# Kernel tuning notes

Hardware: AMD Instinct MI355X
Metric: run time of the kernel (lower is better)

## Reference

```python
import jax, jax.numpy as jnp
import numpy as np

N = 50000          # num nodes
E_RAND = 1_600_000 # random edges (self-loops appended -> E = E_RAND + N)
H, D = 4, 32       # heads, per-head dim
HID = H * D        # 128
L = 3              # num GATv2 layers
NODE_DIM, GRAPH_DIM = 64, 32
EPS = 1e-5


def setup_inputs() -> dict:
    key = jax.random.key(0)
    ks = jax.random.split(key, 24)
    s = 0.05  # param init scale
    node_feats = jax.random.normal(ks[0], (N, NODE_DIM), jnp.float32)
    graph_feats = jax.random.normal(ks[1], (GRAPH_DIM,), jnp.float32)
    # random edges + self loops (mirrors dgl.add_self_loop in forward)
    src = jnp.concatenate([jax.random.randint(ks[2], (E_RAND,), 0, N), jnp.arange(N)]).astype(jnp.int32)
    dst = jnp.concatenate([jax.random.randint(ks[3], (E_RAND,), 0, N), jnp.arange(N)]).astype(jnp.int32)
    p = lambda k, shp: s * jax.random.normal(k, shp, jnp.float32)
    return {
        'node_feats': node_feats, 'graph_feats': graph_feats, 'src': src, 'dst': dst,
        'W_in': p(ks[4], (NODE_DIM, HID)), 'b_in': jnp.zeros((HID,), jnp.float32),
        'W_g': p(ks[5], (GRAPH_DIM, HID)), 'b_g': jnp.zeros((HID,), jnp.float32),
        'W_src': p(ks[6], (L, HID, HID)), 'b_src': jnp.zeros((L, HID), jnp.float32),
        'W_dst': p(ks[7], (L, HID, HID)), 'b_dst': jnp.zeros((L, HID), jnp.float32),
        'attn': p(ks[8], (L, H, D)),
        'ln_g': jnp.ones((L, HID), jnp.float32), 'ln_b': jnp.zeros((L, HID), jnp.float32),
        'W_f1': p(ks[9], (2 * HID, HID)), 'b_f1': jnp.zeros((HID,), jnp.float32),
        'W_f2': p(ks[10], (HID, HID)), 'b_f2': jnp.zeros((HID,), jnp.float32),
    }


def _layernorm(x, g, b):
    m = jnp.mean(x, -1, keepdims=True)
    v = jnp.mean(jnp.square(x - m), -1, keepdims=True)
    return (x - m) * jax.lax.rsqrt(v + EPS) * g + b


def _gatv2(h, src, dst, Ws, bs, Wd, bd, a):
    # DGL GATv2Conv (share_weights=False, residual identity since in==H*D)
    fs = (h @ Ws + bs).reshape(N, H, D)
    fd = (h @ Wd + bd).reshape(N, H, D)
    e = jax.nn.leaky_relu(fs[src] + fd[dst], 0.2)          # [E,H,D]
    logits = jnp.einsum('ehd,hd->eh', e, a)                # [E,H]
    mx = jax.ops.segment_max(logits, dst, num_segments=N)  # [N,H]
    ex = jnp.exp(logits - mx[dst])
    den = jax.ops.segment_sum(ex, dst, num_segments=N)     # [N,H]
    alpha = ex / den[dst]                                  # edge softmax
    out = jax.ops.segment_sum(alpha[:, :, None] * fs[src], dst, num_segments=N)
    return out.reshape(N, HID) + h                         # identity residual


def reference(node_feats, graph_feats, src, dst, W_in, b_in, W_g, b_g,
              W_src, b_src, W_dst, b_dst, attn, ln_g, ln_b,
              W_f1, b_f1, W_f2, b_f2):
    h = node_feats @ W_in + b_in                # [N,HID]
    graph_h = graph_feats @ W_g + b_g           # [HID]
    for l in range(L):
        h_new = _gatv2(h, src, dst, W_src[l], b_src[l], W_dst[l], b_dst[l], attn[l])
        h = jax.nn.relu(_layernorm(h + h_new, ln_g[l], ln_b[l]))  # dropout eval-mode
    pooled = jnp.mean(h, axis=0)                # [HID]
    combined = jnp.concatenate([pooled, graph_h])
    graph_emb = jax.nn.relu(combined @ W_f1 + b_f1) @ W_f2 + b_f2
    return graph_emb, h
```

## Files before the change

### kernel.cpp

```cpp
#include <hip/hip_runtime.h>

typedef unsigned short ushort_t;
typedef unsigned int   uint_t;
typedef unsigned char  uchar_t;
typedef __attribute__((ext_vector_type(8))) __bf16 bf16x8;
typedef __attribute__((ext_vector_type(4))) float   f32x4;

__device__ __forceinline__ float bl(uint_t u){ return __uint_as_float(u<<16); }
__device__ __forceinline__ float bh(uint_t u){ return __uint_as_float(u & 0xffff0000u); }
__device__ __forceinline__ ushort_t f2b(float f){
  uint_t x = __float_as_uint(f);
  return (ushort_t)((x + 0x7fffu + ((x>>16)&1u)) >> 16);
}
__device__ __forceinline__ uint_t pack2(float a, float b){
  return (uint_t)f2b(a) | ((uint_t)f2b(b) << 16);
}

__device__ __forceinline__ float row_reduce16(float p){
  float t;
  t = __uint_as_float(__builtin_amdgcn_update_dpp(0, __float_as_uint(p), 0x121, 0xf, 0xf, true)); p += t;
  t = __uint_as_float(__builtin_amdgcn_update_dpp(0, __float_as_uint(p), 0x122, 0xf, 0xf, true)); p += t;
  t = __uint_as_float(__builtin_amdgcn_update_dpp(0, __float_as_uint(p), 0x124, 0xf, 0xf, true)); p += t;
  t = __uint_as_float(__builtin_amdgcn_update_dpp(0, __float_as_uint(p), 0x128, 0xf, 0xf, true)); p += t;
  return p;
}

#define NBK 128
#define PBLK 256

__global__ __launch_bounds__(256) void k_fuse_a(
    const float* __restrict__ Wsrc, const float* __restrict__ Wdst,
    ushort_t* __restrict__ WB,
    const int* __restrict__ dst, int* __restrict__ bhist, int E, int epb,
    float* __restrict__ pooled)
{
  int blk = blockIdx.x;
  if (blk < 48) {
    int t = blk*256 + threadIdx.x;
    int l = t >> 12;
    int rem = t & 4095;
    int ct = rem >> 8;
    int kc = (rem >> 6) & 3;
    int lane = rem & 63;
    int n = ct*16 + (lane & 15);
    int kbase = kc*32 + (lane >> 4)*8;
    const float* Wp; int nn;
    if (n < 128) { Wp = Wsrc + l*16384; nn = n; }
    else         { Wp = Wdst + l*16384; nn = n - 128; }
    uint4 o;
    o.x = pack2(Wp[(kbase+0)*128+nn], Wp[(kbase+1)*128+nn]);
    o.y = pack2(Wp[(kbase+2)*128+nn], Wp[(kbase+3)*128+nn]);
    o.z = pack2(Wp[(kbase+4)*128+nn], Wp[(kbase+5)*128+nn]);
    o.w = pack2(Wp[(kbase+6)*128+nn], Wp[(kbase+7)*128+nn]);
    *(uint4*)&WB[(size_t)t * 8] = o;
  } else if (blk < 304) {
    __shared__ int lh[NBK];
    int b2 = blk - 48, t = threadIdx.x;
    if (t < NBK) lh[t] = 0;
    __syncthreads();
    int s = b2*epb, e = s + epb; if (e > E) e = E;
    for (int i = s + t; i < e; i += 256)
      atomicAdd(&lh[dst[i] >> 9], 1);
    __syncthreads();
    if (t < NBK) bhist[t*PBLK + b2] = lh[t];
  } else {
    if (threadIdx.x < 128) pooled[threadIdx.x] = 0.f;
  }
}

__global__ __launch_bounds__(1024) void k_scan2(
    const int* __restrict__ bhist, int* __restrict__ gOff,
    int* __restrict__ bucketOff, int E)
{
  __shared__ int sums[1024];
  int tid = threadIdx.x;
  int s0 = tid * 32;
  int local = 0;
  #pragma unroll
  for (int i = 0; i < 32; ++i) local += bhist[s0 + i];
  sums[tid] = local;
  __syncthreads();
  for (int off = 1; off < 1024; off <<= 1) {
    int v = (tid >= off) ? sums[tid - off] : 0;
    __syncthreads();
    sums[tid] += v;
    __syncthreads();
  }
  int run = (tid == 0) ? 0 : sums[tid - 1];
  #pragma unroll
  for (int i = 0; i < 32; ++i) { gOff[s0 + i] = run; run += bhist[s0 + i]; }
  __syncthreads();
  if (tid < NBK) bucketOff[tid] = gOff[tid*PBLK];
  if (tid == NBK) bucketOff[NBK] = E;
}

__global__ __launch_bounds__(256) void k_fuse_b(
    const int* __restrict__ src, const int* __restrict__ dst,
    const int* __restrict__ gOff, uint_t* __restrict__ part, int E, int epb,
    const float* __restrict__ nf, const float* __restrict__ W,
    const float* __restrict__ b, ushort_t* __restrict__ HB, int N)
{
  __shared__ int loff[NBK];
  __shared__ float sA[64*64];
  if (blockIdx.x < PBLK) {
    int blk = blockIdx.x, t = threadIdx.x;
    if (t < NBK) loff[t] = gOff[t*PBLK + blk];
    __syncthreads();
    int s = blk*epb, e = s + epb; if (e > E) e = E;
    for (int i = s + t; i < e; i += 256) {
      int d = dst[i];
      int bb = d >> 9;
      int p = atomicAdd(&loff[bb], 1);
      part[p] = (uint_t)src[i] | ((uint_t)(d & 511) << 16);
    }
  } else {
    int row0 = (blockIdx.x - PBLK) * 64;
    int tid = threadIdx.x;
    {
      int q = tid;
      #pragma unroll
      for (int j = 0; j < 4; ++j, q += 256) {
        int r = q >> 4;
        int c = (q & 15) << 2;
        float4 v = make_float4(0.f,0.f,0.f,0.f);
        if (row0 + r < N) v = *(const float4*)&nf[(size_t)(row0 + r)*64 + c];
        *(float4*)&sA[r*64 + c] = v;
      }
    }
    __syncthreads();
    int cg = tid & 15, rg = tid >> 4;
    int c0 = cg * 8;
    float acc[4][8];
    #pragma unroll
    for (int i = 0; i < 4; ++i)
      #pragma unroll
      for (int j = 0; j < 8; ++j) acc[i][j] = 0.f;
    for (int k = 0; k < 64; ++k) {
      float4 wa = *(const float4*)&W[k*128 + c0];
      float4 wb = *(const float4*)&W[k*128 + c0 + 4];
      float w[8] = {wa.x,wa.y,wa.z,wa.w,wb.x,wb.y,wb.z,wb.w};
      float hv[4];
      #pragma unroll
      for (int i = 0; i < 4; ++i) hv[i] = sA[(rg*4 + i)*64 + k];
      #pragma unroll
      for (int i = 0; i < 4; ++i)
        #pragma unroll
        for (int j = 0; j < 8; ++j) acc[i][j] += hv[i]*w[j];
    }
    float4 b1 = *(const float4*)&b[c0];
    float4 b2 = *(const float4*)&b[c0 + 4];
    float bb[8] = {b1.x,b1.y,b1.z,b1.w,b2.x,b2.y,b2.z,b2.w};
    #pragma unroll
    for (int i = 0; i < 4; ++i) {
      int row = row0 + rg*4 + i;
      if (row < N) {
        uint4 hb;
        hb.x = pack2(acc[i][0]+bb[0], acc[i][1]+bb[1]);
        hb.y = pack2(acc[i][2]+bb[2], acc[i][3]+bb[3]);
        hb.z = pack2(acc[i][4]+bb[4], acc[i][5]+bb[5]);
        hb.w = pack2(acc[i][6]+bb[6], acc[i][7]+bb[7]);
        *(uint4*)&HB[(size_t)row*128 + c0] = hb;
      }
    }
  }
}

__global__ __launch_bounds__(512) void k_csr(
    const uint_t* __restrict__ part, const int* __restrict__ bucketOff,
    int* __restrict__ rowp, int* __restrict__ csrc32, int N, int E)
{
  __shared__ int lcnt[512];
  __shared__ int lpos[512];
  int b = blockIdx.x, t = threadIdx.x;
  int base = b << 9;
  int cnt = N - base; if (cnt > 512) cnt = 512;
  lcnt[t] = 0;
  __syncthreads();
  int s = bucketOff[b], e = bucketOff[b + 1];
  for (int i = s + t; i < e; i += 512)
    atomicAdd(&lcnt[part[i] >> 16], 1);
  __syncthreads();
  int v = lcnt[t];
  lpos[t] = v;
  __syncthreads();
  for (int off = 1; off < 512; off <<= 1) {
    int u = (t >= off) ? lpos[t - off] : 0;
    __syncthreads();
    lpos[t] += u;
    __syncthreads();
  }
  int rp = s + lpos[t] - v;
  if (t < cnt) rowp[base + t] = rp;
  if (b == 0 && t == 0) rowp[N] = E;
  __syncthreads();
  lpos[t] = rp;
  __syncthreads();
  for (int i = s + t; i < e; i += 512) {
    uint_t pr = part[i];
    int p = atomicAdd(&lpos[pr >> 16], 1);
    csrc32[p] = (int)((pr & 0xffffu) << 7);
  }
}

__global__ __launch_bounds__(256) void k_gemm_mfma(
    const ushort_t* __restrict__ HB, const ushort_t* __restrict__ WB,
    const float* __restrict__ bsrc, const float* __restrict__ bdst,
    uchar_t* __restrict__ FS8, ushort_t* __restrict__ FD, int N)
{
  int m0 = blockIdx.x * 32;
  int tid = threadIdx.x;
  int w = tid >> 6, lane = tid & 63;
  int lrow = lane & 15, lk = lane >> 4;

  bf16x8 a[2][4];
  #pragma unroll
  for (int rt = 0; rt < 2; ++rt) {
    int row = m0 + rt*16 + lrow;
    if (row > N-1) row = N-1;
    #pragma unroll
    for (int kc = 0; kc < 4; ++kc)
      a[rt][kc] = *(const bf16x8*)&HB[(size_t)row*128 + kc*32 + lk*8];
  }

  #pragma unroll
  for (int c = 0; c < 4; ++c) {
    int ct = w*4 + c;
    int n = ct*16 + lrow;
    bf16x8 bfr[4];
    #pragma unroll
    for (int kc = 0; kc < 4; ++kc)
      bfr[kc] = *(const bf16x8*)&WB[((size_t)(ct*4 + kc)*64 + lane) * 8];
    if (ct < 8) {
      float bias = bsrc[n];
      #pragma unroll
      for (int rt = 0; rt < 2; ++rt) {
        f32x4 acc = {0.f, 0.f, 0.f, 0.f};
        #pragma unroll
        for (int kc = 0; kc < 4; ++kc)
          acc = __builtin_amdgcn_mfma_f32_16x16x32_bf16(a[rt][kc], bfr[kc], acc, 0, 0, 0);
        int r = m0 + rt*16 + lk*4;
        int w01 = __builtin_amdgcn_cvt_pk_fp8_f32(acc[0]+bias, acc[1]+bias, 0, false);
        int w23 = __builtin_amdgcn_cvt_pk_fp8_f32(acc[2]+bias, acc[3]+bias, 0, false);
        if (r     < N) FS8[(size_t)(r    )*128 + n] = (uchar_t)(w01);
        if (r + 1 < N) FS8[(size_t)(r + 1)*128 + n] = (uchar_t)(w01 >> 8);
        if (r + 2 < N) FS8[(size_t)(r + 2)*128 + n] = (uchar_t)(w23);
        if (r + 3 < N) FS8[(size_t)(r + 3)*128 + n] = (uchar_t)(w23 >> 8);
      }
    } else {
      int nn = n & 127;
      float bias = bdst[nn];
      #pragma unroll
      for (int rt = 0; rt < 2; ++rt) {
        f32x4 acc = {0.f, 0.f, 0.f, 0.f};
        #pragma unroll
        for (int kc = 0; kc < 4; ++kc)
          acc = __builtin_amdgcn_mfma_f32_16x16x32_bf16(a[rt][kc], bfr[kc], acc, 0, 0, 0);
        #pragma unroll
        for (int reg = 0; reg < 4; ++reg) {
          int row = m0 + rt*16 + lk*4 + reg;
          if (row < N) FD[(size_t)row*128 + nn] = f2b(acc[reg] + bias);
        }
      }
    }
  }
}

__global__ __launch_bounds__(256) void k_edge(
    const uchar_t* __restrict__ FS8, const ushort_t* __restrict__ FD,
    ushort_t* __restrict__ HB, float* __restrict__ H,
    const int* __restrict__ rowp, const int* __restrict__ csrc32,
    const float* __restrict__ attn, const float* __restrict__ lng,
    const float* __restrict__ lnb, int last, int N)
{
  int node = __builtin_amdgcn_readfirstlane(blockIdx.x * 4 + (threadIdx.x >> 6));
  if (node >= N) return;
  int lane = threadIdx.x & 63;
  int g = lane >> 4;
  int c = lane & 15;
  int cb = c << 3;

  float fdv[8], av6[8], av4[8];
  {
    uint4 fdu = *(const uint4*)((const char*)FD + node*256 + (cb << 1));
    fdv[0]=bl(fdu.x); fdv[1]=bh(fdu.x); fdv[2]=bl(fdu.y); fdv[3]=bh(fdu.y);
    fdv[4]=bl(fdu.z); fdv[5]=bh(fdu.z); fdv[6]=bl(fdu.w); fdv[7]=bh(fdu.w);
    float4 a1 = *(const float4*)&attn[cb];
    float4 a2 = *(const float4*)&attn[cb + 4];
    float aa[8] = {a1.x,a1.y,a1.z,a1.w,a2.x,a2.y,a2.z,a2.w};
    #pragma unroll
    for (int k = 0; k < 8; ++k) {
      av6[k] = aa[k] * 0.865617024f;
      av4[k] = aa[k] * 0.577078016f;
    }
  }
  int beg = __builtin_amdgcn_readfirstlane(rowp[node]);
  int end = __builtin_amdgcn_readfirstlane(rowp[node + 1]);
  int deg = end - beg;
  int npair = deg >> 4, ntail = deg & 15;
  int tb = beg + (npair << 4);
  int endm1 = end - 1;

  float den = 0.f;
  float acc[8];
  #pragma unroll
  for (int k = 0; k < 8; ++k) acc[k] = 0.f;

  uint2 a0,a1q,a2q,a3q, b0,b1q,b2q,b3q, t0,t1q,t2q,t3q;

  #define PREF(bu0, bu1, kb) {                                              \
    int s0 = csrc32[(kb) + g];                                              \
    int s1 = csrc32[(kb) + 4 + g];                                          \
    bu0 = *(const uint2*)((const char*)FS8 + s0 + cb);                      \
    bu1 = *(const uint2*)((const char*)FS8 + s1 + cb);                      \
  }

  #define PREFT(bu0, bu1, kb) {                                             \
    int i0 = (kb) + g;     i0 = (i0 < endm1) ? i0 : endm1;                  \
    int i1 = (kb) + 4 + g; i1 = (i1 < endm1) ? i1 : endm1;                  \
    bu0 = *(const uint2*)((const char*)FS8 + csrc32[i0] + cb);              \
    bu1 = *(const uint2*)((const char*)FS8 + csrc32[i1] + cb);              \
  }

  #define QM(u, MASKED, kbq) {                                              \
    float cf[8];                                                            \
    { auto p01 = __builtin_amdgcn_cvt_pk_f32_fp8((int)(u).x, false);        \
      auto p23 = __builtin_amdgcn_cvt_pk_f32_fp8((int)(u).x, true);         \
      auto p45 = __builtin_amdgcn_cvt_pk_f32_fp8((int)(u).y, false);        \
      auto p67 = __builtin_amdgcn_cvt_pk_f32_fp8((int)(u).y, true);         \
      cf[0]=p01[0]; cf[1]=p01[1]; cf[2]=p23[0]; cf[3]=p23[1];               \
      cf[4]=p45[0]; cf[5]=p45[1]; cf[6]=p67[0]; cf[7]=p67[1]; }             \
    float p = 0.f;                                                          \
    _Pragma("unroll")                                                       \
    for (int k = 0; k < 8; ++k) {                                           \
      float x = cf[k] + fdv[k];                                             \
      p = fmaf(x, av6[k], p);                                               \
      p = fmaf(fabsf(x), av4[k], p);                                        \
    }                                                                       \
    p = row_reduce16(p);                                                    \
    float ex = __builtin_amdgcn_exp2f(p);                                   \
    if (MASKED) ex = ((kbq) + g < end) ? ex : 0.f;                          \
    den += ex;                                                              \
    _Pragma("unroll")                                                       \
    for (int k = 0; k < 8; ++k) acc[k] = fmaf(ex, cf[k], acc[k]);           \
  }

  if (ntail) { PREFT(t0, t1q, tb) PREFT(t2q, t3q, tb + 8) }
  if (npair) {
    PREF(a0, a1q, beg) PREF(a2q, a3q, beg + 8)
    int rem2 = npair, kb = beg + 16;
    for (;;) {
      if (rem2 > 1) { PREF(b0, b1q, kb) PREF(b2q, b3q, kb + 8) }
      QM(a0, 0, 0) QM(a1q, 0, 0) QM(a2q, 0, 0) QM(a3q, 0, 0)
      if (--rem2 == 0) break;
      kb += 16;
      if (rem2 > 1) { PREF(a0, a1q, kb) PREF(a2q, a3q, kb + 8) }
      QM(b0, 0, 0) QM(b1q, 0, 0) QM(b2q, 0, 0) QM(b3q, 0, 0)
      if (--rem2 == 0) break;
      kb += 16;
    }
  }
  if (ntail) {
    QM(t0, 1, tb) QM(t1q, 1, tb + 4) QM(t2q, 1, tb + 8) QM(t3q, 1, tb + 12)
  }
  #undef PREF
  #undef PREFT
  #undef QM

  den += __shfl_xor(den, 16); den += __shfl_xor(den, 32);
  #pragma unroll
  for (int k = 0; k < 8; ++k) {
    acc[k] += __shfl_xor(acc[k], 16);
    acc[k] += __shfl_xor(acc[k], 32);
  }
  float rden = 1.f / den;

  float x[8];
  {
    uint4 hu = *(const uint4*)((const char*)HB + node*256 + (cb << 1));
    float hb[8] = {bl(hu.x),bh(hu.x),bl(hu.y),bh(hu.y),
                   bl(hu.z),bh(hu.z),bl(hu.w),bh(hu.w)};
    #pragma unroll
    for (int k = 0; k < 8; ++k) x[k] = 2.f*hb[k] + acc[k]*rden;
  }
  float s = 0.f;
  #pragma unroll
  for (int k = 0; k < 8; ++k) s += x[k];
  s = row_reduce16(s);
  float mean = s * (1.f/128.f);
  float v = 0.f;
  #pragma unroll
  for (int k = 0; k < 8; ++k) { x[k] -= mean; v += x[k]*x[k]; }
  v = row_reduce16(v);
  float rs = rsqrtf(v * (1.f/128.f) + 1e-5f);
  float4 g1 = *(const float4*)&lng[cb];
  float4 g2 = *(const float4*)&lng[cb + 4];
  float4 be1 = *(const float4*)&lnb[cb];
  float4 be2 = *(const float4*)&lnb[cb + 4];
  float gv[8] = {g1.x,g1.y,g1.z,g1.w,g2.x,g2.y,g2.z,g2.w};
  float bv[8] = {be1.x,be1.y,be1.z,be1.w,be2.x,be2.y,be2.z,be2.w};
  float y[8];
  #pragma unroll
  for (int k = 0; k < 8; ++k) y[k] = fmaxf(x[k]*rs*gv[k] + bv[k], 0.f);

  if (lane < 16) {
    if (last) {
      float4 o1 = make_float4(y[0],y[1],y[2],y[3]);
      float4 o2 = make_float4(y[4],y[5],y[6],y[7]);
      *(float4*)((char*)H + node*512 + (cb << 2))      = o1;
      *(float4*)((char*)H + node*512 + (cb << 2) + 16) = o2;
    } else {
      uint4 o;
      o.x = pack2(y[0],y[1]); o.y = pack2(y[2],y[3]);
      o.z = pack2(y[4],y[5]); o.w = pack2(y[6],y[7]);
      *(uint4*)((char*)HB + node*256 + (cb << 1)) = o;
    }
  }
}

__global__ __launch_bounds__(128) void k_pool(const float* __restrict__ H,
                                              float* __restrict__ pooled, int N){
  int c = threadIdx.x;
  float s = 0.f;
  for (int r = blockIdx.x; r < N; r += gridDim.x) s += H[(size_t)r*128 + c];
  atomicAdd(&pooled[c], s);
}

__global__ __launch_bounds__(256) void k_final(
    const float* __restrict__ gf, const float* __restrict__ pooled,
    const float* __restrict__ Wg, const float* __restrict__ bg,
    const float* __restrict__ Wf1, const float* __restrict__ bf1,
    const float* __restrict__ Wf2, const float* __restrict__ bf2v,
    float* __restrict__ out, float inv_n)
{
  __shared__ float comb[256];
  __shared__ float t1[128];
  int tid = threadIdx.x;
  if (tid < 128) {
    comb[tid] = pooled[tid] * inv_n;
  } else {
    int c = tid - 128;
    float s = bg[c];
    for (int k = 0; k < 32; ++k) s += gf[k] * Wg[k*128 + c];
    comb[128 + c] = s;
  }
  __syncthreads();
  if (tid < 128) {
    float s = bf1[tid];
    for (int k = 0; k < 256; ++k) s += comb[k] * Wf1[k*128 + tid];
    t1[tid] = fmaxf(s, 0.f);
  }
  __syncthreads();
  if (tid < 128) {
    float s = bf2v[tid];
    for (int k = 0; k < 128; ++k) s += t1[k] * Wf2[k*128 + tid];
    out[tid] = s;
  }
}

extern "C" void kernel_launch(void* const* d_in, const int* in_sizes, int n_in,
                              void* d_out, int out_size, void* d_ws, size_t ws_size,
                              hipStream_t stream) {
  const float* node_feats = (const float*)d_in[0];
  const float* graph_feats= (const float*)d_in[1];
  const int*   src        = (const int*)d_in[2];
  const int*   dst        = (const int*)d_in[3];
  const float* W_in  = (const float*)d_in[4];
  const float* b_in  = (const float*)d_in[5];
  const float* W_g   = (const float*)d_in[6];
  const float* b_g   = (const float*)d_in[7];
  const float* W_src = (const float*)d_in[8];
  const float* b_src = (const float*)d_in[9];
  const float* W_dst = (const float*)d_in[10];
  const float* b_dst = (const float*)d_in[11];
  const float* attn  = (const float*)d_in[12];
  const float* ln_g  = (const float*)d_in[13];
  const float* ln_b  = (const float*)d_in[14];
  const float* W_f1  = (const float*)d_in[15];
  const float* b_f1  = (const float*)d_in[16];
  const float* W_f2  = (const float*)d_in[17];
  const float* b_f2  = (const float*)d_in[18];

  int N = in_sizes[0] / 64;
  int E = in_sizes[2];

  float* out_f = (float*)d_out;
  float* GEMB  = out_f;
  float* H     = out_f + 128;

  float*    pooled = (float*)d_ws;
  uchar_t*  FS8 = (uchar_t*)((char*)d_ws + 512);
  ushort_t* FD = (ushort_t*)(FS8 + (size_t)N * 128);
  ushort_t* HB = FD + (size_t)N * 128;
  ushort_t* WB = HB + (size_t)N * 128;
  int* ibase = (int*)(WB + 3*32768);
  int* rowp      = ibase;
  int* bhist     = ibase + N + 1;
  int* gOff      = bhist + NBK*PBLK;
  int* bucketOff = gOff + NBK*PBLK;
  int* csrc32    = bucketOff + NBK + 1;
  uint_t* part   = (uint_t*)FS8;

  int epb = (E + PBLK - 1) / PBLK;
  int nb  = (N + 511) >> 9;
  int gemm_in_blocks = (N + 63) / 64;

  k_fuse_a<<<305, 256, 0, stream>>>(W_src, W_dst, WB, dst, bhist, E, epb, pooled);
  k_scan2<<<1, 1024, 0, stream>>>(bhist, gOff, bucketOff, E);
  k_fuse_b<<<PBLK + gemm_in_blocks, 256, 0, stream>>>(
      src, dst, gOff, part, E, epb, node_feats, W_in, b_in, HB, N);
  k_csr<<<nb, 512, 0, stream>>>(part, bucketOff, rowp, csrc32, N, E);

  for (int l = 0; l < 3; ++l) {
    k_gemm_mfma<<<(N + 31)/32, 256, 0, stream>>>(
        HB, WB + (size_t)l*32768, b_src + l*128, b_dst + l*128, FS8, FD, N);
    k_edge<<<(N + 3)/4, 256, 0, stream>>>(
        FS8, FD, HB, H, rowp, csrc32,
        attn + l*128, ln_g + l*128, ln_b + l*128, (l == 2) ? 1 : 0, N);
  }

  k_pool<<<512, 128, 0, stream>>>(H, pooled, N);
  k_final<<<1, 256, 0, stream>>>(graph_feats, pooled, W_g, b_g, W_f1, b_f1,
                                 W_f2, b_f2, GEMB, 1.0f / (float)N);
}
```

Baseline: 352.9 us.

## Fuse CSR build with first-layer GEMM, deepen edge prefetch, shrink buckets

Moves the edge-partition buffer into the output H region so the CSR-building blocks can run in the same launch as the layer-0 projection GEMM. The new fused kernel assigns its first blocks to CSR construction and the rest to the GEMM, which removes one launch and lets the two overlap. Buckets are narrowed from 512 to 256 nodes (256 buckets), so CSR blocks use 256 threads. The edge kernel drops to 2 nodes per 128-thread block and triple-buffers its gathers. Risks include more register pressure from the extra buffers and the bucket/partition bookkeeping depending on N fitting the 256-bucket layout.

```diff
diff --git a/kernel.cpp b/kernel.cpp
--- a/kernel.cpp
+++ b/kernel.cpp
@@ -25,7 +25,7 @@
   return p;
 }
 
-#define NBK 128
+#define NBK 256
 #define PBLK 256
 
 __global__ __launch_bounds__(256) void k_fuse_a(
@@ -56,13 +56,13 @@
   } else if (blk < 304) {
     __shared__ int lh[NBK];
     int b2 = blk - 48, t = threadIdx.x;
-    if (t < NBK) lh[t] = 0;
+    lh[t] = 0;
     __syncthreads();
     int s = b2*epb, e = s + epb; if (e > E) e = E;
     for (int i = s + t; i < e; i += 256)
-      atomicAdd(&lh[dst[i] >> 9], 1);
-    __syncthreads();
-    if (t < NBK) bhist[t*PBLK + b2] = lh[t];
+      atomicAdd(&lh[dst[i] >> 8], 1);
+    __syncthreads();
+    bhist[t*PBLK + b2] = lh[t];
   } else {
     if (threadIdx.x < 128) pooled[threadIdx.x] = 0.f;
   }
@@ -74,10 +74,10 @@
 {
   __shared__ int sums[1024];
   int tid = threadIdx.x;
-  int s0 = tid * 32;
+  int s0 = tid * 64;
   int local = 0;
   #pragma unroll
-  for (int i = 0; i < 32; ++i) local += bhist[s0 + i];
+  for (int i = 0; i < 64; ++i) local += bhist[s0 + i];
   sums[tid] = local;
   __syncthreads();
   for (int off = 1; off < 1024; off <<= 1) {
@@ -88,7 +88,7 @@
   }
   int run = (tid == 0) ? 0 : sums[tid - 1];
   #pragma unroll
-  for (int i = 0; i < 32; ++i) { gOff[s0 + i] = run; run += bhist[s0 + i]; }
+  for (int i = 0; i < 64; ++i) { gOff[s0 + i] = run; run += bhist[s0 + i]; }
   __syncthreads();
   if (tid < NBK) bucketOff[tid] = gOff[tid*PBLK];
   if (tid == NBK) bucketOff[NBK] = E;
@@ -104,14 +104,14 @@
   __shared__ float sA[64*64];
   if (blockIdx.x < PBLK) {
     int blk = blockIdx.x, t = threadIdx.x;
-    if (t < NBK) loff[t] = gOff[t*PBLK + blk];
+    loff[t] = gOff[t*PBLK + blk];
     __syncthreads();
     int s = blk*epb, e = s + epb; if (e > E) e = E;
     for (int i = s + t; i < e; i += 256) {
       int d = dst[i];
-      int bb = d >> 9;
+      int bb = d >> 8;
       int p = atomicAdd(&loff[bb], 1);
-      part[p] = (uint_t)src[i] | ((uint_t)(d & 511) << 16);
+      part[p] = (uint_t)src[i] | ((uint_t)(d & 255) << 16);
     }
   } else {
     int row0 = (blockIdx.x - PBLK) * 64;
@@ -165,50 +165,12 @@
   }
 }
 
-__global__ __launch_bounds__(512) void k_csr(
-    const uint_t* __restrict__ part, const int* __restrict__ bucketOff,
-    int* __restrict__ rowp, int* __restrict__ csrc32, int N, int E)
-{
-  __shared__ int lcnt[512];
-  __shared__ int lpos[512];
-  int b = blockIdx.x, t = threadIdx.x;
-  int base = b << 9;
-  int cnt = N - base; if (cnt > 512) cnt = 512;
-  lcnt[t] = 0;
-  __syncthreads();
-  int s = bucketOff[b], e = bucketOff[b + 1];
-  for (int i = s + t; i < e; i += 512)
-    atomicAdd(&lcnt[part[i] >> 16], 1);
-  __syncthreads();
-  int v = lcnt[t];
-  lpos[t] = v;
-  __syncthreads();
-  for (int off = 1; off < 512; off <<= 1) {
-    int u = (t >= off) ? lpos[t - off] : 0;
-    __syncthreads();
-    lpos[t] += u;
-    __syncthreads();
-  }
-  int rp = s + lpos[t] - v;
-  if (t < cnt) rowp[base + t] = rp;
-  if (b == 0 && t == 0) rowp[N] = E;
-  __syncthreads();
-  lpos[t] = rp;
-  __syncthreads();
-  for (int i = s + t; i < e; i += 512) {
-    uint_t pr = part[i];
-    int p = atomicAdd(&lpos[pr >> 16], 1);
-    csrc32[p] = (int)((pr & 0xffffu) << 7);
-  }
-}
-
-__global__ __launch_bounds__(256) void k_gemm_mfma(
-    const ushort_t* __restrict__ HB, const ushort_t* __restrict__ WB,
+__device__ __forceinline__ void gemm_body(
+    int tile, const ushort_t* __restrict__ HB, const ushort_t* __restrict__ WB,
     const float* __restrict__ bsrc, const float* __restrict__ bdst,
-    uchar_t* __restrict__ FS8, ushort_t* __restrict__ FD, int N)
-{
-  int m0 = blockIdx.x * 32;
-  int tid = threadIdx.x;
+    uchar_t* __restrict__ FS8, ushort_t* __restrict__ FD, int N, int tid)
+{
+  int m0 = tile * 32;
   int w = tid >> 6, lane = tid & 63;
   int lrow = lane & 15, lk = lane >> 4;
 
@@ -265,14 +227,66 @@
   }
 }
 
-__global__ __launch_bounds__(256) void k_edge(
+__global__ __launch_bounds__(256) void k_gemm_mfma(
+    const ushort_t* __restrict__ HB, const ushort_t* __restrict__ WB,
+    const float* __restrict__ bsrc, const float* __restrict__ bdst,
+    uchar_t* __restrict__ FS8, ushort_t* __restrict__ FD, int N)
+{
+  gemm_body(blockIdx.x, HB, WB, bsrc, bdst, FS8, FD, N, threadIdx.x);
+}
+
+__global__ __launch_bounds__(256) void k_fuse_c(
+    const uint_t* __restrict__ part, const int* __restrict__ bucketOff,
+    int* __restrict__ rowp, int* __restrict__ csrc32, int N, int E, int nb,
+    const ushort_t* __restrict__ HB, const ushort_t* __restrict__ WB,
+    const float* __restrict__ bsrc, const float* __restrict__ bdst,
+    uchar_t* __restrict__ FS8, ushort_t* __restrict__ FD)
+{
+  if ((int)blockIdx.x < nb) {
+    __shared__ int lcnt[256];
+    __shared__ int lpos[256];
+    int b = blockIdx.x, t = threadIdx.x;
+    int base = b << 8;
+    int cnt = N - base; if (cnt > 256) cnt = 256;
+    lcnt[t] = 0;
+    __syncthreads();
+    int s = bucketOff[b], e = bucketOff[b + 1];
+    for (int i = s + t; i < e; i += 256)
+      atomicAdd(&lcnt[part[i] >> 16], 1);
+    __syncthreads();
+    int v = lcnt[t];
+    lpos[t] = v;
+    __syncthreads();
+    for (int off = 1; off < 256; off <<= 1) {
+      int u = (t >= off) ? lpos[t - off] : 0;
+      __syncthreads();
+      lpos[t] += u;
+      __syncthreads();
+    }
+    int rp = s + lpos[t] - v;
+    if (t < cnt) rowp[base + t] = rp;
+    if (b == 0 && t == 0) rowp[N] = E;
+    __syncthreads();
+    lpos[t] = rp;
+    __syncthreads();
+    for (int i = s + t; i < e; i += 256) {
+      uint_t pr = part[i];
+      int p = atomicAdd(&lpos[pr >> 16], 1);
+      csrc32[p] = (int)((pr & 0xffffu) << 7);
+    }
+  } else {
+    gemm_body(blockIdx.x - nb, HB, WB, bsrc, bdst, FS8, FD, N, threadIdx.x);
+  }
+}
+
+__global__ __launch_bounds__(128) void k_edge(
     const uchar_t* __restrict__ FS8, const ushort_t* __restrict__ FD,
     ushort_t* __restrict__ HB, float* __restrict__ H,
     const int* __restrict__ rowp, const int* __restrict__ csrc32,
     const float* __restrict__ attn, const float* __restrict__ lng,
     const float* __restrict__ lnb, int last, int N)
 {
-  int node = __builtin_amdgcn_readfirstlane(blockIdx.x * 4 + (threadIdx.x >> 6));
+  int node = __builtin_amdgcn_readfirstlane(blockIdx.x * 2 + (threadIdx.x >> 6));
   if (node >= N) return;
   int lane = threadIdx.x & 63;
   int g = lane >> 4;
@@ -305,20 +319,17 @@
   #pragma unroll
   for (int k = 0; k < 8; ++k) acc[k] = 0.f;
 
-  uint2 a0,a1q,a2q,a3q, b0,b1q,b2q,b3q, t0,t1q,t2q,t3q;
-
-  #define PREF(bu0, bu1, kb) {                                              \
+  uint2 A0,A1,A2,A3, B0,B1,B2,B3, C0,C1,C2,C3, T0,T1,T2,T3;
+
+  #define PREF16(x0,x1,x2,x3, kb) {                                         \
     int s0 = csrc32[(kb) + g];                                              \
     int s1 = csrc32[(kb) + 4 + g];                                          \
-    bu0 = *(const uint2*)((const char*)FS8 + s0 + cb);                      \
-    bu1 = *(const uint2*)((const char*)FS8 + s1 + cb);                      \
-  }
-
-  #define PREFT(bu0, bu1, kb) {                                             \
-    int i0 = (kb) + g;     i0 = (i0 < endm1) ? i0 : endm1;                  \
-    int i1 = (kb) + 4 + g; i1 = (i1 < endm1) ? i1 : endm1;                  \
-    bu0 = *(const uint2*)((const char*)FS8 + csrc32[i0] + cb);              \
-    bu1 = *(const uint2*)((const char*)FS8 + csrc32[i1] + cb);              \
+    int s2 = csrc32[(kb) + 8 + g];                                          \
+    int s3 = csrc32[(kb) + 12 + g];                                         \
+    x0 = *(const uint2*)((const char*)FS8 + s0 + cb);                       \
+    x1 = *(const uint2*)((const char*)FS8 + s1 + cb);                       \
+    x2 = *(const uint2*)((const char*)FS8 + s2 + cb);                       \
+    x3 = *(const uint2*)((const char*)FS8 + s3 + cb);                       \
   }
 
   #define QM(u, MASKED, kbq) {                                              \
@@ -344,26 +355,39 @@
     for (int k = 0; k < 8; ++k) acc[k] = fmaf(ex, cf[k], acc[k]);           \
   }
 
-  if (ntail) { PREFT(t0, t1q, tb) PREFT(t2q, t3q, tb + 8) }
+  if (ntail) {
+    int i0 = tb + g;      i0 = (i0 < endm1) ? i0 : endm1;
+    int i1 = tb + 4 + g;  i1 = (i1 < endm1) ? i1 : endm1;
+    int i2 = tb + 8 + g;  i2 = (i2 < endm1) ? i2 : endm1;
+    int i3 = tb + 12 + g; i3 = (i3 < endm1) ? i3 : endm1;
+    T0 = *(const uint2*)((const char*)FS8 + csrc32[i0] + cb);
+    T1 = *(const uint2*)((const char*)FS8 + csrc32[i1] + cb);
+    T2 = *(const uint2*)((const char*)FS8 + csrc32[i2] + cb);
+    T3 = *(const uint2*)((const char*)FS8 + csrc32[i3] + cb);
+  }
   if (npair) {
-    PREF(a0, a1q, beg) PREF(a2q, a3q, beg + 8)
-    int rem2 = npair, kb = beg + 16;
+    PREF16(A0,A1,A2,A3, beg)
+    if (npair > 1) { PREF16(B0,B1,B2,B3, beg + 16) }
+    int rem2 = npair, kb = beg + 32;
     for (;;) {
-      if (rem2 > 1) { PREF(b0, b1q, kb) PREF(b2q, b3q, kb + 8) }
-      QM(a0, 0, 0) QM(a1q, 0, 0) QM(a2q, 0, 0) QM(a3q, 0, 0)
+      if (rem2 > 2) { PREF16(C0,C1,C2,C3, kb) }
+      QM(A0, 0, 0) QM(A1, 0, 0) QM(A2, 0, 0) QM(A3, 0, 0)
       if (--rem2 == 0) break;
       kb += 16;
-      if (rem2 > 1) { PREF(a0, a1q, kb) PREF(a2q, a3q, kb + 8) }
-      QM(b0, 0, 0) QM(b1q, 0, 0) QM(b2q, 0, 0) QM(b3q, 0, 0)
+      if (rem2 > 2) { PREF16(A0,A1,A2,A3, kb) }
+      QM(B0, 0, 0) QM(B1, 0, 0) QM(B2, 0, 0) QM(B3, 0, 0)
       if (--rem2 == 0) break;
       kb += 16;
+      if (rem2 > 2) { PREF16(B0,B1,B2,B3, kb) }
+      QM(C0, 0, 0) QM(C1, 0, 0) QM(C2, 0, 0) QM(C3, 0, 0)
+      if (--rem2 == 0) break;
+      kb += 16;
     }
   }
   if (ntail) {
-    QM(t0, 1, tb) QM(t1q, 1, tb + 4) QM(t2q, 1, tb + 8) QM(t3q, 1, tb + 12)
-  }
-  #undef PREF
-  #undef PREFT
+    QM(T0, 1, tb) QM(T1, 1, tb + 4) QM(T2, 1, tb + 8) QM(T3, 1, tb + 12)
+  }
+  #undef PREF16
   #undef QM
 
   den += __shfl_xor(den, 16); den += __shfl_xor(den, 32);
@@ -498,22 +522,28 @@
   int* gOff      = bhist + NBK*PBLK;
   int* bucketOff = gOff + NBK*PBLK;
   int* csrc32    = bucketOff + NBK + 1;
-  uint_t* part   = (uint_t*)FS8;
+  uint_t* part   = (uint_t*)H;
 
   int epb = (E + PBLK - 1) / PBLK;
-  int nb  = (N + 511) >> 9;
+  int nb  = (N + 255) >> 8;
   int gemm_in_blocks = (N + 63) / 64;
+  int gemm_blocks    = (N + 31) / 32;
 
   k_fuse_a<<<305, 256, 0, stream>>>(W_src, W_dst, WB, dst, bhist, E, epb, pooled);
   k_scan2<<<1, 1024, 0, stream>>>(bhist, gOff, bucketOff, E);
   k_fuse_b<<<PBLK + gemm_in_blocks, 256, 0, stream>>>(
       src, dst, gOff, part, E, epb, node_feats, W_in, b_in, HB, N);
-  k_csr<<<nb, 512, 0, stream>>>(part, bucketOff, rowp, csrc32, N, E);
-
-  for (int l = 0; l < 3; ++l) {
-    k_gemm_mfma<<<(N + 31)/32, 256, 0, stream>>>(
+  k_fuse_c<<<nb + gemm_blocks, 256, 0, stream>>>(
+      part, bucketOff, rowp, csrc32, N, E, nb,
+      HB, WB, b_src, b_dst, FS8, FD);
+  k_edge<<<(N + 1)/2, 128, 0, stream>>>(
+      FS8, FD, HB, H, rowp, csrc32,
+      attn, ln_g, ln_b, 0, N);
+
+  for (int l = 1; l < 3; ++l) {
+    k_gemm_mfma<<<gemm_blocks, 256, 0, stream>>>(
         HB, WB + (size_t)l*32768, b_src + l*128, b_dst + l*128, FS8, FD, N);
-    k_edge<<<(N + 3)/4, 256, 0, stream>>>(
+    k_edge<<<(N + 1)/2, 128, 0, stream>>>(
         FS8, FD, HB, H, rowp, csrc32,
         attn + l*128, ln_g + l*128, ln_b + l*128, (l == 2) ? 1 : 0, N);
   }
```

Measured after the change: 357.9 us. Within noise of the previous version (+1.4%).

## Store dst features in fp8 and CSR source indices as 16-bit

Applied to the files above, without the earlier changes.

The GEMM now writes the destination projection FD as fp8, the same way as FS, instead of bf16, and the edge kernel decodes it with packed fp8 converts. CSR source indices are stored as 16-bit node ids and shifted at load time instead of as prescaled 32-bit offsets. This halves the bytes for FD and for the per-edge index stream in the edge kernel. The cost is lower precision in the attention logits, and a 16-bit index only holds while N stays at or below 65536.

```diff
diff --git a/kernel.cpp b/kernel.cpp
--- a/kernel.cpp
+++ b/kernel.cpp
@@ -167,7 +167,7 @@
 
 __global__ __launch_bounds__(512) void k_csr(
     const uint_t* __restrict__ part, const int* __restrict__ bucketOff,
-    int* __restrict__ rowp, int* __restrict__ csrc32, int N, int E)
+    int* __restrict__ rowp, ushort_t* __restrict__ csrc16, int N, int E)
 {
   __shared__ int lcnt[512];
   __shared__ int lpos[512];
@@ -198,14 +198,14 @@
   for (int i = s + t; i < e; i += 512) {
     uint_t pr = part[i];
     int p = atomicAdd(&lpos[pr >> 16], 1);
-    csrc32[p] = (int)((pr & 0xffffu) << 7);
+    csrc16[p] = (ushort_t)(pr & 0xffffu);
   }
 }
 
 __global__ __launch_bounds__(256) void k_gemm_mfma(
     const ushort_t* __restrict__ HB, const ushort_t* __restrict__ WB,
     const float* __restrict__ bsrc, const float* __restrict__ bdst,
-    uchar_t* __restrict__ FS8, ushort_t* __restrict__ FD, int N)
+    uchar_t* __restrict__ FS8, uchar_t* __restrict__ FD8, int N)
 {
   int m0 = blockIdx.x * 32;
   int tid = threadIdx.x;
@@ -230,45 +230,30 @@
     #pragma unroll
     for (int kc = 0; kc < 4; ++kc)
       bfr[kc] = *(const bf16x8*)&WB[((size_t)(ct*4 + kc)*64 + lane) * 8];
-    if (ct < 8) {
-      float bias = bsrc[n];
+    int nn = n & 127;
+    uchar_t* OUT = (ct < 8) ? FS8 : FD8;
+    float bias = (ct < 8) ? bsrc[nn] : bdst[nn];
+    #pragma unroll
+    for (int rt = 0; rt < 2; ++rt) {
+      f32x4 acc = {0.f, 0.f, 0.f, 0.f};
       #pragma unroll
-      for (int rt = 0; rt < 2; ++rt) {
-        f32x4 acc = {0.f, 0.f, 0.f, 0.f};
-        #pragma unroll
-        for (int kc = 0; kc < 4; ++kc)
-          acc = __builtin_amdgcn_mfma_f32_16x16x32_bf16(a[rt][kc], bfr[kc], acc, 0, 0, 0);
-        int r = m0 + rt*16 + lk*4;
-        int w01 = __builtin_amdgcn_cvt_pk_fp8_f32(acc[0]+bias, acc[1]+bias, 0, false);
-        int w23 = __builtin_amdgcn_cvt_pk_fp8_f32(acc[2]+bias, acc[3]+bias, 0, false);
-        if (r     < N) FS8[(size_t)(r    )*128 + n] = (uchar_t)(w01);
-        if (r + 1 < N) FS8[(size_t)(r + 1)*128 + n] = (uchar_t)(w01 >> 8);
-        if (r + 2 < N) FS8[(size_t)(r + 2)*128 + n] = (uchar_t)(w23);
-        if (r + 3 < N) FS8[(size_t)(r + 3)*128 + n] = (uchar_t)(w23 >> 8);
-      }
-    } else {
-      int nn = n & 127;
-      float bias = bdst[nn];
-      #pragma unroll
-      for (int rt = 0; rt < 2; ++rt) {
-        f32x4 acc = {0.f, 0.f, 0.f, 0.f};
-        #pragma unroll
-        for (int kc = 0; kc < 4; ++kc)
-          acc = __builtin_amdgcn_mfma_f32_16x16x32_bf16(a[rt][kc], bfr[kc], acc, 0, 0, 0);
-        #pragma unroll
-        for (int reg = 0; reg < 4; ++reg) {
-          int row = m0 + rt*16 + lk*4 + reg;
-          if (row < N) FD[(size_t)row*128 + nn] = f2b(acc[reg] + bias);
-        }
-      }
+      for (int kc = 0; kc < 4; ++kc)
+        acc = __builtin_amdgcn_mfma_f32_16x16x32_bf16(a[rt][kc], bfr[kc], acc, 0, 0, 0);
+      int r = m0 + rt*16 + lk*4;
+      int w01 = __builtin_amdgcn_cvt_pk_fp8_f32(acc[0]+bias, acc[1]+bias, 0, false);
+      int w23 = __builtin_amdgcn_cvt_pk_fp8_f32(acc[2]+bias, acc[3]+bias, 0, false);
+      if (r     < N) OUT[(size_t)(r    )*128 + nn] = (uchar_t)(w01);
+      if (r + 1 < N) OUT[(size_t)(r + 1)*128 + nn] = (uchar_t)(w01 >> 8);
+      if (r + 2 < N) OUT[(size_t)(r + 2)*128 + nn] = (uchar_t)(w23);
+      if (r + 3 < N) OUT[(size_t)(r + 3)*128 + nn] = (uchar_t)(w23 >> 8);
     }
   }
 }
 
 __global__ __launch_bounds__(256) void k_edge(
-    const uchar_t* __restrict__ FS8, const ushort_t* __restrict__ FD,
+    const uchar_t* __restrict__ FS8, const uchar_t* __restrict__ FD8,
     ushort_t* __restrict__ HB, float* __restrict__ H,
-    const int* __restrict__ rowp, const int* __restrict__ csrc32,
+    const int* __restrict__ rowp, const ushort_t* __restrict__ csrc16,
     const float* __restrict__ attn, const float* __restrict__ lng,
     const float* __restrict__ lnb, int last, int N)
 {
@@ -281,9 +266,13 @@
 
   float fdv[8], av6[8], av4[8];
   {
-    uint4 fdu = *(const uint4*)((const char*)FD + node*256 + (cb << 1));
-    fdv[0]=bl(fdu.x); fdv[1]=bh(fdu.x); fdv[2]=bl(fdu.y); fdv[3]=bh(fdu.y);
-    fdv[4]=bl(fdu.z); fdv[5]=bh(fdu.z); fdv[6]=bl(fdu.w); fdv[7]=bh(fdu.w);
+    uint2 fdu = *(const uint2*)((const char*)FD8 + node*128 + cb);
+    auto f01 = __builtin_amdgcn_cvt_pk_f32_fp8((int)fdu.x, false);
+    auto f23 = __builtin_amdgcn_cvt_pk_f32_fp8((int)fdu.x, true);
+    auto f45 = __builtin_amdgcn_cvt_pk_f32_fp8((int)fdu.y, false);
+    auto f67 = __builtin_amdgcn_cvt_pk_f32_fp8((int)fdu.y, true);
+    fdv[0]=f01[0]; fdv[1]=f01[1]; fdv[2]=f23[0]; fdv[3]=f23[1];
+    fdv[4]=f45[0]; fdv[5]=f45[1]; fdv[6]=f67[0]; fdv[7]=f67[1];
     float4 a1 = *(const float4*)&attn[cb];
     float4 a2 = *(const float4*)&attn[cb + 4];
     float aa[8] = {a1.x,a1.y,a1.z,a1.w,a2.x,a2.y,a2.z,a2.w};
@@ -308,8 +297,8 @@
   uint2 a0,a1q,a2q,a3q, b0,b1q,b2q,b3q, t0,t1q,t2q,t3q;
 
   #define PREF(bu0, bu1, kb) {                                              \
-    int s0 = csrc32[(kb) + g];                                              \
-    int s1 = csrc32[(kb) + 4 + g];                                          \
+    int s0 = ((int)csrc16[(kb) + g]) << 7;                                  \
+    int s1 = ((int)csrc16[(kb) + 4 + g]) << 7;                              \
     bu0 = *(const uint2*)((const char*)FS8 + s0 + cb);                      \
     bu1 = *(const uint2*)((const char*)FS8 + s1 + cb);                      \
   }
@@ -317,8 +306,8 @@
   #define PREFT(bu0, bu1, kb) {                                             \
     int i0 = (kb) + g;     i0 = (i0 < endm1) ? i0 : endm1;                  \
     int i1 = (kb) + 4 + g; i1 = (i1 < endm1) ? i1 : endm1;                  \
-    bu0 = *(const uint2*)((const char*)FS8 + csrc32[i0] + cb);              \
-    bu1 = *(const uint2*)((const char*)FS8 + csrc32[i1] + cb);              \
+    bu0 = *(const uint2*)((const char*)FS8 + (((int)csrc16[i0]) << 7) + cb);\
+    bu1 = *(const uint2*)((const char*)FS8 + (((int)csrc16[i1]) << 7) + cb);\
   }
 
   #define QM(u, MASKED, kbq) {                                              \
@@ -489,15 +478,15 @@
 
   float*    pooled = (float*)d_ws;
   uchar_t*  FS8 = (uchar_t*)((char*)d_ws + 512);
-  ushort_t* FD = (ushort_t*)(FS8 + (size_t)N * 128);
-  ushort_t* HB = FD + (size_t)N * 128;
-  ushort_t* WB = HB + (size_t)N * 128;
+  uchar_t*  FD8 = FS8 + (size_t)N * 128;
+  ushort_t* HB  = (ushort_t*)(FD8 + (size_t)N * 128);
+  ushort_t* WB  = HB + (size_t)N * 128;
   int* ibase = (int*)(WB + 3*32768);
   int* rowp      = ibase;
   int* bhist     = ibase + N + 1;
   int* gOff      = bhist + NBK*PBLK;
   int* bucketOff = gOff + NBK*PBLK;
-  int* csrc32    = bucketOff + NBK + 1;
+  ushort_t* csrc16 = (ushort_t*)(bucketOff + NBK + 1);
   uint_t* part   = (uint_t*)FS8;
 
   int epb = (E + PBLK - 1) / PBLK;
@@ -508,13 +497,13 @@
   k_scan2<<<1, 1024, 0, stream>>>(bhist, gOff, bucketOff, E);
   k_fuse_b<<<PBLK + gemm_in_blocks, 256, 0, stream>>>(
       src, dst, gOff, part, E, epb, node_feats, W_in, b_in, HB, N);
-  k_csr<<<nb, 512, 0, stream>>>(part, bucketOff, rowp, csrc32, N, E);
+  k_csr<<<nb, 512, 0, stream>>>(part, bucketOff, rowp, csrc16, N, E);
 
   for (int l = 0; l < 3; ++l) {
     k_gemm_mfma<<<(N + 31)/32, 256, 0, stream>>>(
-        HB, WB + (size_t)l*32768, b_src + l*128, b_dst + l*128, FS8, FD, N);
+        HB, WB + (size_t)l*32768, b_src + l*128, b_dst + l*128, FS8, FD8, N);
     k_edge<<<(N + 3)/4, 256, 0, stream>>>(
-        FS8, FD, HB, H, rowp, csrc32,
+        FS8, FD8, HB, H, rowp, csrc16,
         attn + l*128, ln_g + l*128, ln_b + l*128, (l == 2) ? 1 : 0, N);
   }
 
```

After: 351.7 us, median of 2. About the same (-0.4%).
